# Kernel optimization log

Measured on AMD Instinct MI355X. Metric: run time of the kernel, lower is better.

Reference implementation:

```python
import jax, jax.numpy as jnp
import numpy as np

B, L, D_IN, D, P, NL = 8, 4096, 64, 512, 512, 3
EPS = 1e-5


def _ln(x, w, b):
    m = x.mean(-1, keepdims=True)
    v = ((x - m) ** 2).mean(-1, keepdims=True)
    return (x - m) * jax.lax.rsqrt(v + EPS) * w + b


def _gelu(x):
    return jax.nn.gelu(x, approximate=False)  # torch default = exact erf GELU


def _s5_scan(u, lam_re, lam_im, Bre, Bim, Cre, Cim, Dp, log_step):
    # u: (L, D). Diagonal complex SSM with ZOH discretization.
    lam = lam_re + 1j * lam_im                      # (P,)
    step = jnp.exp(log_step)                        # (P,)
    lam_bar = jnp.exp(lam * step)                   # (P,)
    Bt = Bre + 1j * Bim                             # (P, D)
    B_bar = ((lam_bar - 1.0) / lam)[:, None] * Bt   # (P, D)
    Bu = u.astype(jnp.complex64) @ B_bar.T          # (L, P)
    A = jnp.broadcast_to(lam_bar, Bu.shape)         # (L, P)

    def binop(a, b):
        A1, b1 = a
        A2, b2 = b
        return (A2 * A1, A2 * b1 + b2)

    _, xs = jax.lax.associative_scan(binop, (A, Bu))  # (L, P) states
    Ct = Cre + 1j * Cim                               # (D, P)
    return 2.0 * jnp.real(xs @ Ct.T) + Dp * u          # (L, D)


def setup_inputs() -> dict:
    key = jax.random.key(0)
    ks = iter(jax.random.split(key, 32))
    r = lambda s, sc=1.0: sc * jax.random.normal(next(ks), s, dtype=jnp.float32)
    inp = {}
    inp['x'] = r((B, L, D_IN))
    inp['lengths'] = jax.random.randint(next(ks), (B,), 1, L + 1, dtype=jnp.int32)
    inp['enc_w'] = r((D_IN, D), 0.05)
    inp['enc_b'] = jnp.zeros((D,), jnp.float32)
    # S5 SSM params per layer (stacked over NL)
    inp['lam_re'] = -jnp.exp(r((NL, P), 0.5))          # stable: Re(Lambda) < 0
    inp['lam_im'] = np.pi * r((NL, P))
    inp['Bre'] = r((NL, P, D), 1.0 / np.sqrt(D))
    inp['Bim'] = r((NL, P, D), 1.0 / np.sqrt(D))
    inp['Cre'] = r((NL, D, P), 1.0 / np.sqrt(P))
    inp['Cim'] = r((NL, D, P), 1.0 / np.sqrt(P))
    inp['Dp'] = r((NL, D))
    inp['log_step'] = jax.random.uniform(next(ks), (NL, P), jnp.float32, np.log(1e-3), np.log(1e-1))
    # S5Block norms and GEGLU FFN (ff_enc: D->2D no bias, ff_dec: D->D no bias)
    inp['an_w'] = jnp.ones((NL, D), jnp.float32)
    inp['an_b'] = jnp.zeros((NL, D), jnp.float32)
    inp['fn_w'] = jnp.ones((NL, D), jnp.float32)
    inp['fn_b'] = jnp.zeros((NL, D), jnp.float32)
    inp['ffe_w'] = r((NL, 2 * D, D), 1.0 / np.sqrt(D))
    inp['ffd_w'] = r((NL, D, D), 1.0 / np.sqrt(D))
    # outer prenorm LayerNorms
    inp['norm_w'] = jnp.ones((NL, D), jnp.float32)
    inp['norm_b'] = jnp.zeros((NL, D), jnp.float32)
    inp['head_w'] = r((1, D), 0.05)
    inp['head_b'] = jnp.zeros((1,), jnp.float32)
    return inp


def reference(x, lengths, enc_w, enc_b, lam_re, lam_im, Bre, Bim, Cre, Cim, Dp,
              log_step, an_w, an_b, fn_w, fn_b, ffe_w, ffd_w, norm_w, norm_b,
              head_w, head_b):
    h = x @ enc_w + enc_b  # (B, L, D)
    s5_b = jax.vmap(_s5_scan, in_axes=(0, None, None, None, None, None, None, None, None))
    for i in range(NL):
        z = _ln(h, norm_w[i], norm_b[i])  # prenorm (dropout = identity in eval)
        # --- S5Block ---
        fx = _ln(z, an_w[i], an_b[i])
        z = _gelu(s5_b(fx, lam_re[i], lam_im[i], Bre[i], Bim[i], Cre[i], Cim[i], Dp[i], log_step[i])) + fx
        fx = _ln(z, fn_w[i], fn_b[i])
        e = fx @ ffe_w[i].T                      # (B, L, 2D)
        a, g = jnp.split(e, 2, axis=-1)
        z = (a * _gelu(g)) @ ffd_w[i].T + fx      # GEGLU + residual
        h = h + z
    mask = (jnp.arange(L)[None, :] < lengths[:, None])[..., None]  # (B, L, 1)
    pooled = (h * mask).sum(axis=1) / jnp.maximum(lengths, 1)[:, None].astype(h.dtype)
    return (pooled @ head_w.T + head_b).squeeze(-1)  # (B,)
```

## Files before the change

### kernel.cpp

```cpp
#include <hip/hip_runtime.h>
#include <hip/hip_bf16.h>
#include <stdint.h>

#define BB 8
#define LL 4096
#define D_IN 64
#define DD 512
#define PP 512
#define NL 3
#define MTOK (BB * LL)
#define SCHUNK 128
#define NCHUNK (LL / SCHUNK)

typedef __bf16 bf16x8 __attribute__((ext_vector_type(8)));
typedef __bf16 bf16x4 __attribute__((ext_vector_type(4)));
typedef float f32x4 __attribute__((ext_vector_type(4)));
typedef float f32x16 __attribute__((ext_vector_type(16)));

typedef const __attribute__((address_space(1))) void gvoid_t;
typedef __attribute__((address_space(3))) void svoid_t;

__device__ __forceinline__ void async16(const __bf16* g, __bf16* l) {
    __builtin_amdgcn_global_load_lds((gvoid_t*)g, (svoid_t*)l, 16, 0, 0);
}

__device__ __forceinline__ float gelu_f(float x) {
    return 0.5f * x * (1.0f + erff(x * 0.70710678118654752440f));
}
__device__ __forceinline__ float wred(float v) {
#pragma unroll
    for (int o = 32; o > 0; o >>= 1) v += __shfl_xor(v, o, 64);
    return v;
}
__device__ __forceinline__ float bflo(uint32_t u) { return __builtin_bit_cast(float, (uint32_t)(u << 16)); }
__device__ __forceinline__ float bfhi(uint32_t u) { return __builtin_bit_cast(float, (uint32_t)(u & 0xffff0000u)); }
__device__ __forceinline__ uint32_t packbf2(float a, float b) {
    unsigned short ha = __builtin_bit_cast(unsigned short, (__bf16)a);
    unsigned short hb = __builtin_bit_cast(unsigned short, (__bf16)b);
    return (uint32_t)ha | ((uint32_t)hb << 16);
}
__device__ __forceinline__ float ldf(const void* p, long i, int f) {
    return f ? ((const float*)p)[i] : (float)((const __bf16*)p)[i];
}
__device__ __forceinline__ void split1(float v, __bf16& h, __bf16& l) {
    h = (__bf16)v;
    l = (__bf16)(v - (float)h);
}

__global__ void detect(const uint32_t* __restrict__ an_w_raw, int* __restrict__ flag) {
    if (threadIdx.x == 0) *flag = (an_w_raw[0] == 0x3F800000u) ? 1 : 0;
}

template <int MODE>
__global__ __launch_bounds__(256) void gemm_bt(
    const __bf16* __restrict__ Ah, const __bf16* __restrict__ Al, int lda,
    const __bf16* __restrict__ Bh, const __bf16* __restrict__ Bl,
    int M, int N, int K,
    __bf16* outh, __bf16* outl, float* h32,
    __bf16* fxh, __bf16* fxl, const float* __restrict__ vec,
    const int* __restrict__ lengths, float* __restrict__ partials, int b0)
{
    __shared__ __attribute__((aligned(16))) char smem[35840];
    __bf16* sAh = (__bf16*)smem;
    __bf16* sAl = (__bf16*)(smem + 8192);
    __bf16* sBh = (__bf16*)(smem + 16384);
    __bf16* sBl = (__bf16*)(smem + 24576);

    const int tid = threadIdx.x;
    const int lane = tid & 63;
    const int wave = tid >> 6;
    const int wm = wave & 1, wn = wave >> 1;
    const long m0 = (long)blockIdx.x * 128;
    const long n0 = (long)blockIdx.y * 128;

    f32x16 acc[2][2] = {};

    const int sr = lane >> 2;
    const int sc = (lane & 3) * 8;
    const long ga = (m0 + wave * 32 + sr) * (long)lda + sc;
    const long gb = (n0 + wave * 32 + sr) * (long)K + sc;
    __bf16* dAh = sAh + wave * 1024;
    __bf16* dAl = sAl + wave * 1024;
    __bf16* dBh = sBh + wave * 1024;
    __bf16* dBl = sBl + wave * 1024;

    const int frow = lane & 31;
    const int fcol = (lane >> 5) * 8;

    for (int k0 = 0; k0 < K; k0 += 32) {
        async16(Ah + ga + k0, dAh);
        async16(Ah + ga + k0 + 16 * (long)lda, dAh + 512);
        async16(Al + ga + k0, dAl);
        async16(Al + ga + k0 + 16 * (long)lda, dAl + 512);
        async16(Bh + gb + k0, dBh);
        async16(Bh + gb + k0 + 16 * (long)K, dBh + 512);
        async16(Bl + gb + k0, dBl);
        async16(Bl + gb + k0 + 16 * (long)K, dBl + 512);
        __syncthreads();
#pragma unroll
        for (int ks = 0; ks < 2; ks++) {
            const int co = ks * 16 + fcol;
            bf16x8 ah[2], al[2], bh[2], bl[2];
#pragma unroll
            for (int t = 0; t < 2; t++) {
                ah[t] = *(const bf16x8*)(sAh + (wm * 64 + t * 32 + frow) * 32 + co);
                al[t] = *(const bf16x8*)(sAl + (wm * 64 + t * 32 + frow) * 32 + co);
                bh[t] = *(const bf16x8*)(sBh + (wn * 64 + t * 32 + frow) * 32 + co);
                bl[t] = *(const bf16x8*)(sBl + (wn * 64 + t * 32 + frow) * 32 + co);
            }
#pragma unroll
            for (int ti = 0; ti < 2; ti++)
#pragma unroll
                for (int tj = 0; tj < 2; tj++) {
                    acc[ti][tj] = __builtin_amdgcn_mfma_f32_32x32x16_bf16(ah[ti], bl[tj], acc[ti][tj], 0, 0, 0);
                    acc[ti][tj] = __builtin_amdgcn_mfma_f32_32x32x16_bf16(al[ti], bh[tj], acc[ti][tj], 0, 0, 0);
                    acc[ti][tj] = __builtin_amdgcn_mfma_f32_32x32x16_bf16(ah[ti], bh[tj], acc[ti][tj], 0, 0, 0);
                }
        }
        __syncthreads();
    }

    float* scratch = (float*)(smem + wave * 8960);
    const int cdc = lane & 31;
    const int rbase = 4 * (lane >> 5);
    const int lr_rd = lane >> 3;
    const int lc_rd = (lane & 7) * 8;

    float pacc = 0.f;
    int lenb = 0;
    if (MODE == 5) lenb = lengths[b0 + (int)(blockIdx.x >> 5)];

#pragma unroll
    for (int g = 0; g < 2; g++) {
#pragma unroll
        for (int tj = 0; tj < 2; tj++)
#pragma unroll
            for (int r = 0; r < 16; r++) {
                const int row = (r & 3) + 8 * (r >> 2) + rbase;
                scratch[row * 68 + tj * 32 + cdc] = acc[g][tj][r];
            }
        __syncthreads();
#pragma unroll
        for (int s = 0; s < 4; s++) {
            const int lr = s * 8 + lr_rd;
            float v8[8];
            *(f32x4*)v8       = *(const f32x4*)&scratch[lr * 68 + lc_rd];
            *(f32x4*)(v8 + 4) = *(const f32x4*)&scratch[lr * 68 + lc_rd + 4];
            const long gm = m0 + wm * 64 + g * 32 + lr;
            const int gc = (int)n0 + wn * 64 + lc_rd;
            if (MODE == 0) {
                const long idx = gm * N + gc;
                bf16x8 h8, l8;
#pragma unroll
                for (int e = 0; e < 8; e++) { __bf16 h, l; split1(v8[e], h, l); h8[e] = h; l8[e] = l; }
                *(bf16x8*)(outh + idx) = h8;
                *(bf16x8*)(outl + idx) = l8;
            } else if (MODE == 1) {
                const long idx = gm * N + gc;
                f32x4 o0, o1;
#pragma unroll
                for (int e = 0; e < 4; e++) { o0[e] = v8[e] + vec[gc + e]; o1[e] = v8[4 + e] + vec[gc + 4 + e]; }
                *(f32x4*)(h32 + idx) = o0;
                *(f32x4*)(h32 + idx + 4) = o1;
            } else if (MODE == 2) {
                const long idx = gm * N + gc;
                const bf16x8 uh = *(const bf16x8*)(fxh + idx);
                const bf16x8 ul = *(const bf16x8*)(fxl + idx);
                bf16x8 h8, l8;
#pragma unroll
                for (int e = 0; e < 8; e++) {
                    const float u = (float)uh[e] + (float)ul[e];
                    const float z = gelu_f(v8[e] + vec[gc + e] * u) + u;
                    __bf16 h, l; split1(z, h, l); h8[e] = h; l8[e] = l;
                }
                *(bf16x8*)(fxh + idx) = h8;
                *(bf16x8*)(fxl + idx) = l8;
            } else if (MODE == 3 || MODE == 5) {
                const long idx = gm * N + gc;
                const bf16x8 uh = *(const bf16x8*)(fxh + idx);
                const bf16x8 ul = *(const bf16x8*)(fxl + idx);
                f32x4 o0 = *(const f32x4*)(h32 + idx);
                f32x4 o1 = *(const f32x4*)(h32 + idx + 4);
#pragma unroll
                for (int e = 0; e < 4; e++) {
                    o0[e] += v8[e] + (float)uh[e] + (float)ul[e];
                    o1[e] += v8[4 + e] + (float)uh[4 + e] + (float)ul[4 + e];
                }
                if (MODE == 3) {
                    *(f32x4*)(h32 + idx) = o0;
                    *(f32x4*)(h32 + idx + 4) = o1;
                } else {
                    if ((int)(gm & (LL - 1)) < lenb) {
#pragma unroll
                        for (int e = 0; e < 4; e++)
                            pacc += o0[e] * vec[gc + e] + o1[e] * vec[gc + 4 + e];
                    }
                }
            } else {
                const long tidx = gm * (N / 2) + (gc >> 1);
                bf16x4 h4, l4;
#pragma unroll
                for (int q = 0; q < 4; q++) {
                    const float t = v8[2 * q] * gelu_f(v8[2 * q + 1]);
                    __bf16 h, l; split1(t, h, l); h4[q] = h; l4[q] = l;
                }
                *(bf16x4*)(outh + tidx) = h4;
                *(bf16x4*)(outl + tidx) = l4;
            }
        }
        __syncthreads();
    }

    if (MODE == 5) {
        pacc = wred(pacc);
        float* red = (float*)smem;
        if (lane == 0) red[wave] = pacc;
        __syncthreads();
        if (tid == 0)
            partials[(long)(b0 + (int)(blockIdx.x >> 5)) * 128 +
                     (int)(blockIdx.x & 31) * 4 + (int)blockIdx.y] =
                red[0] + red[1] + red[2] + red[3];
    }
}

template <bool DBL, bool F32IN>
__global__ __launch_bounds__(256) void ln_kernel(
    const float* __restrict__ xf, const __bf16* xh, const __bf16* xl,
    __bf16* oh, __bf16* ol,
    const float* __restrict__ w1, const float* __restrict__ b1,
    const float* __restrict__ w2, const float* __restrict__ b2)
{
    const int lane = threadIdx.x & 63;
    const int wave = threadIdx.x >> 6;
    const long row = (long)blockIdx.x * 4 + wave;
    const int c0 = lane * 8;

    float v[8];
    if (F32IN) {
        const float* xp = xf + row * DD + c0;
        const float4 a = *(const float4*)xp;
        const float4 b = *(const float4*)(xp + 4);
        v[0] = a.x; v[1] = a.y; v[2] = a.z; v[3] = a.w;
        v[4] = b.x; v[5] = b.y; v[6] = b.z; v[7] = b.w;
    } else {
        const bf16x8 a = *(const bf16x8*)(xh + row * DD + c0);
        const bf16x8 b = *(const bf16x8*)(xl + row * DD + c0);
#pragma unroll
        for (int j = 0; j < 8; j++) v[j] = (float)a[j] + (float)b[j];
    }

    float s = 0.f;
#pragma unroll
    for (int j = 0; j < 8; j++) s += v[j];
    s = wred(s);
    float m = s * (1.0f / DD);
    float q = 0.f;
#pragma unroll
    for (int j = 0; j < 8; j++) { const float d = v[j] - m; q += d * d; }
    q = wred(q);
    float rstd = rsqrtf(q * (1.0f / DD) + 1e-5f);
    float y[8];
#pragma unroll
    for (int j = 0; j < 8; j++)
        y[j] = (v[j] - m) * rstd * w1[c0 + j] + b1[c0 + j];

    if (DBL) {
        s = 0.f;
#pragma unroll
        for (int j = 0; j < 8; j++) s += y[j];
        s = wred(s);
        m = s * (1.0f / DD);
        q = 0.f;
#pragma unroll
        for (int j = 0; j < 8; j++) { const float d = y[j] - m; q += d * d; }
        q = wred(q);
        rstd = rsqrtf(q * (1.0f / DD) + 1e-5f);
#pragma unroll
        for (int j = 0; j < 8; j++)
            y[j] = (y[j] - m) * rstd * w2[c0 + j] + b2[c0 + j];
    }

    bf16x8 oh8, ol8;
#pragma unroll
    for (int j = 0; j < 8; j++) { __bf16 h, l; split1(y[j], h, l); oh8[j] = h; ol8[j] = l; }
    *(bf16x8*)(oh + row * DD + c0) = oh8;
    *(bf16x8*)(ol + row * DD + c0) = ol8;
}

__global__ void prep_small(const void* enc_w, __bf16* __restrict__ eh, __bf16* __restrict__ el,
                           const void* lam_re, const void* lam_im, const void* logst,
                           float2* __restrict__ lamb, float2* __restrict__ abars,
                           float2* __restrict__ coef,
                           const void* nw, const void* nb, const void* aw, const void* ab,
                           const void* fw, const void* fb, const void* dp,
                           const void* eb, const void* hw, const void* hb,
                           float* __restrict__ cv, const int* __restrict__ flag)
{
    const int idx = blockIdx.x * 256 + threadIdx.x;
    const int f = *flag;
    {
        const int n = idx >> 6, k = idx & 63;
        __bf16 h, l;
        split1(ldf(enc_w, (long)k * DD + n, f), h, l);
        eh[idx] = h; el[idx] = l;
    }
    if (idx < NL * PP) {
        const float lre = ldf(lam_re, idx, f), lim = ldf(lam_im, idx, f);
        const float st = expf(ldf(logst, idx, f));
        const float ea = expf(lre * st);
        const float ang = lim * st;
        const float br = ea * cosf(ang), bi = ea * sinf(ang);
        lamb[idx] = make_float2(br, bi);
        float ar = br, ai = bi;
#pragma unroll
        for (int q = 0; q < 7; q++) { const float t = ar * ar - ai * ai; ai = 2.f * ar * ai; ar = t; }
        abars[idx] = make_float2(ar, ai);
        const float nr = br - 1.f, ni = bi;
        const float den = lre * lre + lim * lim;
        coef[idx] = make_float2((nr * lre + ni * lim) / den, (ni * lre - nr * lim) / den);
    }
    const int NV = NL * DD;
    if (idx < 7 * NV + 1025) {
        if (idx < NV) cv[idx] = ldf(nw, idx, f);
        else if (idx < 2 * NV) cv[idx] = ldf(nb, idx - NV, f);
        else if (idx < 3 * NV) cv[idx] = ldf(aw, idx - 2 * NV, f);
        else if (idx < 4 * NV) cv[idx] = ldf(ab, idx - 3 * NV, f);
        else if (idx < 5 * NV) cv[idx] = ldf(fw, idx - 4 * NV, f);
        else if (idx < 6 * NV) cv[idx] = ldf(fb, idx - 5 * NV, f);
        else if (idx < 7 * NV) cv[idx] = ldf(dp, idx - 6 * NV, f);
        else if (idx < 7 * NV + 512) cv[idx] = ldf(eb, idx - 7 * NV, f);
        else if (idx < 7 * NV + 1024) cv[idx] = ldf(hw, idx - 7 * NV - 512, f);
        else cv[idx] = ldf(hb, idx - 7 * NV - 1024, f);
    }
}

__global__ void prep_w12(const void* Bre, const void* Bim, const float2* __restrict__ coef,
                         __bf16* __restrict__ W1th, __bf16* __restrict__ W1tl,
                         const void* Cre, const void* Cim,
                         __bf16* __restrict__ W2th, __bf16* __restrict__ W2tl,
                         const int* __restrict__ flag)
{
    const long idx = (long)blockIdx.x * 256 + threadIdx.x;
    const int f = *flag;
    const long li = idx >> 18;
    const int pd = (int)(idx & ((1 << 18) - 1));
    {
        const int p = pd >> 9, d = pd & 511;
        const float2 c = coef[li * PP + p];
        const float br = ldf(Bre, idx, f), bi = ldf(Bim, idx, f);
        const float re = c.x * br - c.y * bi;
        const float im = c.x * bi + c.y * br;
        const long base = li * (2 * PP) * DD;
        __bf16 h, l;
        split1(re, h, l); W1th[base + (long)(2 * p) * DD + d] = h; W1tl[base + (long)(2 * p) * DD + d] = l;
        split1(im, h, l); W1th[base + (long)(2 * p + 1) * DD + d] = h; W1tl[base + (long)(2 * p + 1) * DD + d] = l;
    }
    {
        const int d = pd >> 9, p = pd & 511;
        const long base = li * DD * (2 * PP);
        __bf16 h, l;
        split1(2.f * ldf(Cre, idx, f), h, l);
        W2th[base + (long)d * (2 * PP) + 2 * p] = h; W2tl[base + (long)d * (2 * PP) + 2 * p] = l;
        split1(-2.f * ldf(Cim, idx, f), h, l);
        W2th[base + (long)d * (2 * PP) + 2 * p + 1] = h; W2tl[base + (long)d * (2 * PP) + 2 * p + 1] = l;
    }
}

__global__ void prep_ff(const void* ffe, __bf16* __restrict__ feh, __bf16* __restrict__ fel,
                        const void* ffd, __bf16* __restrict__ fdh, __bf16* __restrict__ fdl,
                        const int* __restrict__ flag)
{
    const long idx = (long)blockIdx.x * 256 + threadIdx.x;
    const int f = *flag;
    {
        const long li = idx >> 19;
        const int rc = (int)(idx & ((1 << 19) - 1));
        const int r = rc >> 9, c = rc & 511;
        const int nr = (r < 512) ? (2 * r) : (2 * (r - 512) + 1);
        __bf16 h, l;
        split1(ldf(ffe, idx, f), h, l);
        const long dst = li * (1 << 19) + (long)nr * 512 + c;
        feh[dst] = h; fel[dst] = l;
    }
    if (idx < (long)NL * DD * DD) {
        __bf16 h, l;
        split1(ldf(ffd, idx, f), h, l);
        fdh[idx] = h; fdl[idx] = l;
    }
}

__global__ void split_arr(const void* src, __bf16* __restrict__ dh, __bf16* __restrict__ dl,
                          long n, const int* __restrict__ flag)
{
    const long idx = (long)blockIdx.x * 256 + threadIdx.x;
    if (idx >= n) return;
    __bf16 h, l;
    split1(ldf(src, idx, *flag), h, l);
    dh[idx] = h; dl[idx] = l;
}

__global__ __launch_bounds__(256) void scan_ends(const uint32_t* __restrict__ wh32,
                                                 const uint32_t* __restrict__ wl32,
                                                 const float2* __restrict__ lamb,
                                                 float2* __restrict__ ends)
{
    const int idx = blockIdx.x * 256 + threadIdx.x;
    const int p = idx & 511;
    const int c = (idx >> 9) & (NCHUNK - 1);
    const int b = idx >> 14;
    const float2 lb = lamb[p];
    const long base = ((long)(b * LL + c * SCHUNK)) * 512 + p;
    float sr = 0.f, si = 0.f;
    for (int j = 0; j < SCHUNK; j++) {
        const uint32_t uh = wh32[base + (long)j * 512];
        const uint32_t ul = wl32[base + (long)j * 512];
        const float br = bflo(uh) + bflo(ul);
        const float bi = bfhi(uh) + bfhi(ul);
        const float ns = fmaf(lb.x, sr, fmaf(-lb.y, si, br));
        si = fmaf(lb.x, si, fmaf(lb.y, sr, bi));
        sr = ns;
    }
    ends[((long)(b * PP + p)) * NCHUNK + c] = make_float2(sr, si);
}

__global__ __launch_bounds__(256) void scan_carry(const float2* __restrict__ abars,
                                                  float2* __restrict__ ends)
{
    const int idx = blockIdx.x * 256 + threadIdx.x;
    const int p = idx & 511;
    const float2 As = abars[p];
    float2* eb = ends + (long)idx * NCHUNK;
    float cr = 0.f, ci = 0.f;
    for (int c = 0; c < NCHUNK; c++) {
        const float2 e = eb[c];
        eb[c] = make_float2(cr, ci);
        const float nr = As.x * cr - As.y * ci + e.x;
        ci = As.x * ci + As.y * cr + e.y;
        cr = nr;
    }
}

__global__ __launch_bounds__(256) void scan_fix(uint32_t* wh32, uint32_t* wl32,
                                                const float2* __restrict__ lamb,
                                                const float2* __restrict__ ends)
{
    const int idx = blockIdx.x * 256 + threadIdx.x;
    const int p = idx & 511;
    const int c = (idx >> 9) & (NCHUNK - 1);
    const int b = idx >> 14;
    const float2 lb = lamb[p];
    const float2 carry = ends[((long)(b * PP + p)) * NCHUNK + c];
    const long base = ((long)(b * LL + c * SCHUNK)) * 512 + p;
    float sr = carry.x, si = carry.y;
    for (int j = 0; j < SCHUNK; j++) {
        const uint32_t uh = wh32[base + (long)j * 512];
        const uint32_t ul = wl32[base + (long)j * 512];
        const float br = bflo(uh) + bflo(ul);
        const float bi = bfhi(uh) + bfhi(ul);
        const float ns = fmaf(lb.x, sr, fmaf(-lb.y, si, br));
        si = fmaf(lb.x, si, fmaf(lb.y, sr, bi));
        sr = ns;
        const float hr = (float)(__bf16)sr, hi_ = (float)(__bf16)si;
        wh32[base + (long)j * 512] = packbf2(sr, si);
        wl32[base + (long)j * 512] = packbf2(sr - hr, si - hi_);
    }
}

__global__ void pool2(const float* __restrict__ partials, const int* __restrict__ lengths,
                      const float* __restrict__ hb_, void* out, const int* __restrict__ flag)
{
    const int b = threadIdx.x;
    if (b >= BB) return;
    float s = 0.f;
    for (int c = 0; c < 128; c++) s += partials[b * 128 + c];
    const int len = lengths[b] < 1 ? 1 : lengths[b];
    const float val = s / (float)len + hb_[0];
    if (*flag) ((float*)out)[b] = val;
    else ((__bf16*)out)[b] = (__bf16)val;
}

extern "C" void kernel_launch(void* const* d_in, const int* in_sizes, int n_in,
                              void* d_out, int out_size, void* d_ws, size_t ws_size,
                              hipStream_t stream)
{
    const void* x      = d_in[0];
    const int* lengths = (const int*)d_in[1];
    const void* enc_w  = d_in[2];
    const void* enc_b  = d_in[3];
    const void* lam_re = d_in[4];
    const void* lam_im = d_in[5];
    const void* Bre    = d_in[6];
    const void* Bim    = d_in[7];
    const void* Cre    = d_in[8];
    const void* Cim    = d_in[9];
    const void* Dp     = d_in[10];
    const void* logst  = d_in[11];
    const void* an_w   = d_in[12];
    const void* an_b   = d_in[13];
    const void* fn_w   = d_in[14];
    const void* fn_b   = d_in[15];
    const void* ffe    = d_in[16];
    const void* ffd    = d_in[17];
    const void* norm_w = d_in[18];
    const void* norm_b = d_in[19];
    const void* head_w = d_in[20];
    const void* head_b = d_in[21];

    char* w = (char*)d_ws;
    auto alloc = [&](size_t bytes) -> char* {
        char* r = w;
        w += (bytes + 255) & ~(size_t)255;
        return r;
    };
    int* dflag    = (int*)alloc(256);
    __bf16* W1th  = (__bf16*)alloc((size_t)NL * 2 * PP * DD * 2);
    __bf16* W1tl  = (__bf16*)alloc((size_t)NL * 2 * PP * DD * 2);
    __bf16* W2th  = (__bf16*)alloc((size_t)NL * DD * 2 * PP * 2);
    __bf16* W2tl  = (__bf16*)alloc((size_t)NL * DD * 2 * PP * 2);
    __bf16* ffeh  = (__bf16*)alloc((size_t)NL * 2 * DD * DD * 2);
    __bf16* ffel  = (__bf16*)alloc((size_t)NL * 2 * DD * DD * 2);
    __bf16* ffdh  = (__bf16*)alloc((size_t)NL * DD * DD * 2);
    __bf16* ffdl  = (__bf16*)alloc((size_t)NL * DD * DD * 2);
    __bf16* ench  = (__bf16*)alloc((size_t)DD * D_IN * 2);
    __bf16* encl  = (__bf16*)alloc((size_t)DD * D_IN * 2);
    __bf16* xh    = (__bf16*)alloc((size_t)MTOK * D_IN * 2);
    __bf16* xl    = (__bf16*)alloc((size_t)MTOK * D_IN * 2);
    float2* lamb  = (float2*)alloc((size_t)NL * PP * 8);
    float2* abars = (float2*)alloc((size_t)NL * PP * 8);
    float2* coef  = (float2*)alloc((size_t)NL * PP * 8);
    float*  cv    = (float*)alloc((size_t)(7 * NL * DD + 1025) * 4);
    float2* ends  = (float2*)alloc((size_t)BB * PP * NCHUNK * 8);
    float* partials = (float*)alloc((size_t)BB * 128 * 4);
    const size_t fixed = (size_t)(w - (char*)d_ws);

    int NB = BB;
    const size_t per_b = (size_t)LL * DD * 16;
    while (NB > 1 && fixed + (size_t)NB * per_b > ws_size) NB >>= 1;
    float* h32  = (float*)alloc((size_t)NB * LL * DD * 4);
    __bf16* fxh = (__bf16*)alloc((size_t)NB * LL * DD * 2);
    __bf16* fxl = (__bf16*)alloc((size_t)NB * LL * DD * 2);
    __bf16* wh  = (__bf16*)alloc((size_t)NB * LL * 2 * PP * 2);
    __bf16* wl  = (__bf16*)alloc((size_t)NB * LL * 2 * PP * 2);

    const float* cv_nw = cv;
    const float* cv_nb = cv + 1536;
    const float* cv_aw = cv + 3072;
    const float* cv_ab = cv + 4608;
    const float* cv_fw = cv + 6144;
    const float* cv_fb = cv + 7680;
    const float* cv_dp = cv + 9216;
    const float* cv_eb = cv + 10752;
    const float* cv_hw = cv + 11264;
    const float* cv_hb = cv + 11776;

    detect<<<1, 64, 0, stream>>>((const uint32_t*)an_w, dflag);
    prep_small<<<128, 256, 0, stream>>>(enc_w, ench, encl, lam_re, lam_im, logst,
                                        lamb, abars, coef,
                                        norm_w, norm_b, an_w, an_b, fn_w, fn_b, Dp,
                                        enc_b, head_w, head_b, cv, dflag);
    prep_w12<<<(NL * PP * DD) / 256, 256, 0, stream>>>(
        Bre, Bim, coef, W1th, W1tl, Cre, Cim, W2th, W2tl, dflag);
    prep_ff<<<((size_t)NL * 2 * DD * DD) / 256, 256, 0, stream>>>(
        ffe, ffeh, ffel, ffd, ffdh, ffdl, dflag);
    split_arr<<<((size_t)MTOK * D_IN + 255) / 256, 256, 0, stream>>>(
        x, xh, xl, (long)MTOK * D_IN, dflag);

    for (int b0 = 0; b0 < BB; b0 += NB) {
        const int M = NB * LL;
        gemm_bt<1><<<dim3(M / 128, DD / 128), 256, 0, stream>>>(
            xh + (long)b0 * LL * D_IN, xl + (long)b0 * LL * D_IN, D_IN,
            ench, encl, M, DD, D_IN, nullptr, nullptr, h32, nullptr, nullptr, cv_eb,
            nullptr, nullptr, 0);

        for (int li = 0; li < NL; li++) {
            ln_kernel<true, true><<<M / 4, 256, 0, stream>>>(
                h32, nullptr, nullptr, fxh, fxl,
                cv_nw + li * DD, cv_nb + li * DD, cv_aw + li * DD, cv_ab + li * DD);
            gemm_bt<0><<<dim3(M / 128, (2 * PP) / 128), 256, 0, stream>>>(
                fxh, fxl, DD, W1th + (long)li * 2 * PP * DD, W1tl + (long)li * 2 * PP * DD,
                M, 2 * PP, DD, wh, wl, nullptr, nullptr, nullptr, nullptr,
                nullptr, nullptr, 0);
            scan_ends<<<(NB * NCHUNK * PP) / 256, 256, 0, stream>>>(
                (const uint32_t*)wh, (const uint32_t*)wl, lamb + li * PP, ends);
            scan_carry<<<(NB * PP) / 256, 256, 0, stream>>>(abars + li * PP, ends);
            scan_fix<<<(NB * NCHUNK * PP) / 256, 256, 0, stream>>>(
                (uint32_t*)wh, (uint32_t*)wl, lamb + li * PP, ends);
            gemm_bt<2><<<dim3(M / 128, DD / 128), 256, 0, stream>>>(
                wh, wl, 2 * PP, W2th + (long)li * DD * 2 * PP, W2tl + (long)li * DD * 2 * PP,
                M, DD, 2 * PP, nullptr, nullptr, nullptr, fxh, fxl, cv_dp + li * DD,
                nullptr, nullptr, 0);
            ln_kernel<false, false><<<M / 4, 256, 0, stream>>>(
                nullptr, fxh, fxl, fxh, fxl,
                cv_fw + li * DD, cv_fb + li * DD, nullptr, nullptr);
            gemm_bt<4><<<dim3(M / 128, (2 * DD) / 128), 256, 0, stream>>>(
                fxh, fxl, DD, ffeh + (long)li * 2 * DD * DD, ffel + (long)li * 2 * DD * DD,
                M, 2 * DD, DD, wh, wl, nullptr, nullptr, nullptr, nullptr,
                nullptr, nullptr, 0);
            if (li < NL - 1) {
                gemm_bt<3><<<dim3(M / 128, DD / 128), 256, 0, stream>>>(
                    wh, wl, DD, ffdh + (long)li * DD * DD, ffdl + (long)li * DD * DD,
                    M, DD, DD, nullptr, nullptr, h32, fxh, fxl, nullptr,
                    nullptr, nullptr, 0);
            } else {
                gemm_bt<5><<<dim3(M / 128, DD / 128), 256, 0, stream>>>(
                    wh, wl, DD, ffdh + (long)li * DD * DD, ffdl + (long)li * DD * DD,
                    M, DD, DD, nullptr, nullptr, h32, fxh, fxl, cv_hw,
                    lengths, partials, b0);
            }
        }
    }
    pool2<<<1, 64, 0, stream>>>(partials, lengths, cv_hb, d_out, dflag);
}
```

Baseline: 2.194 ms.

## Switch GEMM to 16x16x32 MFMA with swizzled LDS and lighter epilogue

Replaces the 32x32x16 MFMA tiles with 16x16x32 MFMAs over a 4x4 accumulator grid per wave, processing the full K=32 slice in one instruction per tile. LDS stores and reads use an XOR swizzle on the 16-byte column chunk to cut bank conflicts. The epilogue now goes through a smaller per-wave scratch with no block-wide barriers, which lets shared memory shrink to 32 KB. A min-blocks-per-CU hint of 5 is added. Together these aim to raise MFMA throughput and occupancy, at the cost of more MFMA instructions and possible register pressure under the launch bound.

```diff
diff --git a/kernel.cpp b/kernel.cpp
--- a/kernel.cpp
+++ b/kernel.cpp
@@ -15,7 +15,6 @@
 typedef __bf16 bf16x8 __attribute__((ext_vector_type(8)));
 typedef __bf16 bf16x4 __attribute__((ext_vector_type(4)));
 typedef float f32x4 __attribute__((ext_vector_type(4)));
-typedef float f32x16 __attribute__((ext_vector_type(16)));
 
 typedef const __attribute__((address_space(1))) void gvoid_t;
 typedef __attribute__((address_space(3))) void svoid_t;
@@ -52,7 +51,7 @@
 }
 
 template <int MODE>
-__global__ __launch_bounds__(256) void gemm_bt(
+__global__ __launch_bounds__(256, 5) void gemm_bt(
     const __bf16* __restrict__ Ah, const __bf16* __restrict__ Al, int lda,
     const __bf16* __restrict__ Bh, const __bf16* __restrict__ Bl,
     int M, int N, int K,
@@ -60,7 +59,7 @@
     __bf16* fxh, __bf16* fxl, const float* __restrict__ vec,
     const int* __restrict__ lengths, float* __restrict__ partials, int b0)
 {
-    __shared__ __attribute__((aligned(16))) char smem[35840];
+    __shared__ __attribute__((aligned(16))) char smem[32768];
     __bf16* sAh = (__bf16*)smem;
     __bf16* sAl = (__bf16*)(smem + 8192);
     __bf16* sBh = (__bf16*)(smem + 16384);
@@ -73,10 +72,10 @@
     const long m0 = (long)blockIdx.x * 128;
     const long n0 = (long)blockIdx.y * 128;
 
-    f32x16 acc[2][2] = {};
+    f32x4 acc[4][4] = {};
 
     const int sr = lane >> 2;
-    const int sc = (lane & 3) * 8;
+    const int sc = ((lane & 3) ^ ((sr >> 1) & 3)) * 8;
     const long ga = (m0 + wave * 32 + sr) * (long)lda + sc;
     const long gb = (n0 + wave * 32 + sr) * (long)K + sc;
     __bf16* dAh = sAh + wave * 1024;
@@ -84,8 +83,8 @@
     __bf16* dBh = sBh + wave * 1024;
     __bf16* dBl = sBl + wave * 1024;
 
-    const int frow = lane & 31;
-    const int fcol = (lane >> 5) * 8;
+    const int fr = lane & 15;
+    const int co = ((lane >> 4) ^ ((fr >> 1) & 3)) * 8;
 
     for (int k0 = 0; k0 < K; k0 += 32) {
         async16(Ah + ga + k0, dAh);
@@ -97,32 +96,28 @@
         async16(Bl + gb + k0, dBl);
         async16(Bl + gb + k0 + 16 * (long)K, dBl + 512);
         __syncthreads();
-#pragma unroll
-        for (int ks = 0; ks < 2; ks++) {
-            const int co = ks * 16 + fcol;
-            bf16x8 ah[2], al[2], bh[2], bl[2];
-#pragma unroll
-            for (int t = 0; t < 2; t++) {
-                ah[t] = *(const bf16x8*)(sAh + (wm * 64 + t * 32 + frow) * 32 + co);
-                al[t] = *(const bf16x8*)(sAl + (wm * 64 + t * 32 + frow) * 32 + co);
-                bh[t] = *(const bf16x8*)(sBh + (wn * 64 + t * 32 + frow) * 32 + co);
-                bl[t] = *(const bf16x8*)(sBl + (wn * 64 + t * 32 + frow) * 32 + co);
+        bf16x8 afh[4], afl[4], bfh[4], bfl[4];
+#pragma unroll
+        for (int i = 0; i < 4; i++) {
+            afh[i] = *(const bf16x8*)(sAh + (wm * 64 + i * 16 + fr) * 32 + co);
+            afl[i] = *(const bf16x8*)(sAl + (wm * 64 + i * 16 + fr) * 32 + co);
+            bfh[i] = *(const bf16x8*)(sBh + (wn * 64 + i * 16 + fr) * 32 + co);
+            bfl[i] = *(const bf16x8*)(sBl + (wn * 64 + i * 16 + fr) * 32 + co);
+        }
+#pragma unroll
+        for (int i = 0; i < 4; i++)
+#pragma unroll
+            for (int j = 0; j < 4; j++) {
+                acc[i][j] = __builtin_amdgcn_mfma_f32_16x16x32_bf16(afh[i], bfl[j], acc[i][j], 0, 0, 0);
+                acc[i][j] = __builtin_amdgcn_mfma_f32_16x16x32_bf16(afl[i], bfh[j], acc[i][j], 0, 0, 0);
+                acc[i][j] = __builtin_amdgcn_mfma_f32_16x16x32_bf16(afh[i], bfh[j], acc[i][j], 0, 0, 0);
             }
-#pragma unroll
-            for (int ti = 0; ti < 2; ti++)
-#pragma unroll
-                for (int tj = 0; tj < 2; tj++) {
-                    acc[ti][tj] = __builtin_amdgcn_mfma_f32_32x32x16_bf16(ah[ti], bl[tj], acc[ti][tj], 0, 0, 0);
-                    acc[ti][tj] = __builtin_amdgcn_mfma_f32_32x32x16_bf16(al[ti], bh[tj], acc[ti][tj], 0, 0, 0);
-                    acc[ti][tj] = __builtin_amdgcn_mfma_f32_32x32x16_bf16(ah[ti], bh[tj], acc[ti][tj], 0, 0, 0);
-                }
-        }
         __syncthreads();
     }
 
-    float* scratch = (float*)(smem + wave * 8960);
-    const int cdc = lane & 31;
-    const int rbase = 4 * (lane >> 5);
+    float* scratch = (float*)smem + wave * 1088;
+    const int er = (lane >> 4) * 4;
+    const int ec = lane & 15;
     const int lr_rd = lane >> 3;
     const int lc_rd = (lane & 7) * 8;
 
@@ -131,22 +126,19 @@
     if (MODE == 5) lenb = lengths[b0 + (int)(blockIdx.x >> 5)];
 
 #pragma unroll
-    for (int g = 0; g < 2; g++) {
-#pragma unroll
-        for (int tj = 0; tj < 2; tj++)
-#pragma unroll
-            for (int r = 0; r < 16; r++) {
-                const int row = (r & 3) + 8 * (r >> 2) + rbase;
-                scratch[row * 68 + tj * 32 + cdc] = acc[g][tj][r];
-            }
-        __syncthreads();
-#pragma unroll
-        for (int s = 0; s < 4; s++) {
+    for (int i = 0; i < 4; i++) {
+#pragma unroll
+        for (int j = 0; j < 4; j++)
+#pragma unroll
+            for (int r = 0; r < 4; r++)
+                scratch[(er + r) * 68 + j * 16 + ec] = acc[i][j][r];
+#pragma unroll
+        for (int s = 0; s < 2; s++) {
             const int lr = s * 8 + lr_rd;
             float v8[8];
             *(f32x4*)v8       = *(const f32x4*)&scratch[lr * 68 + lc_rd];
             *(f32x4*)(v8 + 4) = *(const f32x4*)&scratch[lr * 68 + lc_rd + 4];
-            const long gm = m0 + wm * 64 + g * 32 + lr;
+            const long gm = m0 + wm * 64 + i * 16 + lr;
             const int gc = (int)n0 + wn * 64 + lc_rd;
             if (MODE == 0) {
                 const long idx = gm * N + gc;
@@ -208,12 +200,11 @@
                 *(bf16x4*)(outl + tidx) = l4;
             }
         }
-        __syncthreads();
     }
 
     if (MODE == 5) {
         pacc = wred(pacc);
-        float* red = (float*)smem;
+        float* red = (float*)(smem + 17408);
         if (lane == 0) red[wave] = pacc;
         __syncthreads();
         if (tid == 0)
```

After: 6.827 ms. 211% more time.
